# Kernel optimization log

Measured on AMD Instinct MI355X. Metric: run time of the kernel, lower is better.

The kernel has to match this reference:

```python
import jax, jax.numpy as jnp
import numpy as np

N_NODES = 50000
N_EDGES = 800000
NUM_GRAPHS = 256
H = 128          # h_dim
C = H + 1        # CGConv channels = 129
Z = 2 * C + 1    # concat(x_i, x_j, edge_attr) = 259
N_GRAPH_LAYERS = 5
N_FC = 3
OUT_DIM = 1


def setup_inputs() -> dict:
    key = jax.random.key(0)
    ks = jax.random.split(key, 12)
    atoms = jax.random.randint(ks[0], (N_NODES,), 0, 119)
    pos = jax.random.normal(ks[1], (N_NODES, 3), dtype=jnp.float32)
    edge_index = jax.random.randint(ks[2], (2, N_EDGES), 0, N_NODES)
    batch = jnp.sort(jax.random.randint(ks[3], (N_NODES,), 0, NUM_GRAPHS))
    s = 0.05
    emb = jax.random.normal(ks[4], (119, H), dtype=jnp.float32)
    Wf = jax.random.normal(ks[5], (N_GRAPH_LAYERS, Z, C), dtype=jnp.float32) * s
    bf = jnp.zeros((N_GRAPH_LAYERS, C), dtype=jnp.float32)
    Ws = jax.random.normal(ks[6], (N_GRAPH_LAYERS, Z, C), dtype=jnp.float32) * s
    bs = jnp.zeros((N_GRAPH_LAYERS, C), dtype=jnp.float32)
    Wfc = jax.random.normal(ks[7], (N_FC, C, C), dtype=jnp.float32) * s
    bfc = jnp.zeros((N_FC, C), dtype=jnp.float32)
    Wout = jax.random.normal(ks[8], (C, OUT_DIM), dtype=jnp.float32) * s
    bout = jnp.zeros((OUT_DIM,), dtype=jnp.float32)
    return {"atoms": atoms, "pos": pos, "edge_index": edge_index, "batch": batch,
            "emb": emb, "Wf": Wf, "bf": bf, "Ws": Ws, "bs": bs,
            "Wfc": Wfc, "bfc": bfc, "Wout": Wout, "bout": bout}


def reference(atoms, pos, edge_index, batch, emb, Wf, bf, Ws, bs, Wfc, bfc, Wout, bout):
    n = atoms.shape[0]
    src, dst = edge_index[0], edge_index[1]  # PyG: x_j = x[src], x_i = x[dst], aggregate at dst
    # edge_attr = ||pos[src] - pos[dst]||, shape [E, 1]
    edge_attr = jnp.linalg.norm(pos[src] - pos[dst], axis=-1, keepdims=True)
    # node features: atom embedding + z-coordinate -> [N, 129]
    x = jnp.concatenate([emb[atoms], pos[:, 2:3]], axis=-1)
    for l in range(Wf.shape[0]):
        z = jnp.concatenate([x[dst], x[src], edge_attr], axis=-1)  # [E, 259]
        m = jax.nn.sigmoid(z @ Wf[l] + bf[l]) * jax.nn.softplus(z @ Ws[l] + bs[l])
        x = x + jax.ops.segment_sum(m, dst, num_segments=n)  # CGConv: aggr='add' + residual
    # mean pooling per graph
    sums = jax.ops.segment_sum(x, batch, num_segments=NUM_GRAPHS)
    cnts = jax.ops.segment_sum(jnp.ones((n, 1), x.dtype), batch, num_segments=NUM_GRAPHS)
    g = sums / jnp.maximum(cnts, 1.0)
    for l in range(Wfc.shape[0]):
        g = g @ Wfc[l] + bfc[l]
    return g @ Wout + bout
```

## Files before the change

### kernel.cpp

```cpp
#include <hip/hip_runtime.h>
#include <math.h>

#define N_NODES 50000
#define N_EDGES 800000
#define NUM_GRAPHS 256
#define NPADROWS 50048
#define CAP 64
#define SCLN -1.44269504088896f
#define SCLP 1.44269504088896f
#define C693 0.69314718056f
#define LROW 264

typedef __attribute__((ext_vector_type(8))) short short8;
typedef __attribute__((ext_vector_type(4))) float f32x4;
typedef __attribute__((ext_vector_type(2))) float f32x2;

__device__ __forceinline__ float fast_rcp(float x) {
#if __has_builtin(__builtin_amdgcn_rcpf)
  return __builtin_amdgcn_rcpf(x);
#else
  return 1.0f / x;
#endif
}
__device__ __forceinline__ float EX2(float x) {
#if __has_builtin(__builtin_amdgcn_exp2f)
  return __builtin_amdgcn_exp2f(x);
#else
  return exp2f(x);
#endif
}
__device__ __forceinline__ float LG2(float x) {
#if __has_builtin(__builtin_amdgcn_logf)
  return __builtin_amdgcn_logf(x);
#else
  return log2f(x);
#endif
}
__device__ __forceinline__ unsigned f2bf(float x) {
  unsigned u = __float_as_uint(x);
  return (u + 0x7fffu + ((u >> 16) & 1u)) >> 16;
}
__device__ __forceinline__ unsigned short bfr(float v) {
  return (unsigned short)((__float_as_uint(v) + 0x8000u) >> 16);
}
__device__ __forceinline__ unsigned pkbfr(float lo, float hi) {
  unsigned a = (__float_as_uint(lo) + 0x8000u) >> 16;
  unsigned b = (__float_as_uint(hi) + 0x8000u) & 0xffff0000u;
  return a | b;
}
__device__ __forceinline__ float u2f(unsigned u) { return __uint_as_float(u); }
__device__ __forceinline__ f32x2 mk2(float a, float b) {
  f32x2 r; r.x = a; r.y = b; return r;
}
__device__ __forceinline__ f32x2 unp(unsigned u) {
  return mk2(u2f(u << 16), u2f(u & 0xffff0000u));
}
__device__ __forceinline__ f32x2 lg2p1(f32x2 t) {
  f32x2 p = __builtin_elementwise_fma(t, (f32x2)0.0439245f, (f32x2)-0.1898214f);
  p = __builtin_elementwise_fma(t, p, (f32x2)0.4115517f);
  p = __builtin_elementwise_fma(t, p, (f32x2)-0.7072504f);
  p = __builtin_elementwise_fma(t, p, (f32x2)1.4415927f);
  return t * p;
}
__device__ __forceinline__ void edge_ch2(f32x2 gf, f32x2 gs, f32x2& acc) {
  f32x2 den = mk2(EX2(gf.x), EX2(gf.y)) + 1.0f;
  f32x2 ts = mk2(EX2(-fabsf(gs.x)), EX2(-fabsf(gs.y)));
  f32x2 sp = lg2p1(ts) + __builtin_elementwise_max(gs, (f32x2)0.0f);
  f32x2 rc = mk2(fast_rcp(den.x), fast_rcp(den.y));
  acc = __builtin_elementwise_fma(rc, sp, acc);
}

__global__ void init_x(const int* __restrict__ atoms, const float* __restrict__ pos,
                       const float* __restrict__ emb, float* __restrict__ x128c,
                       unsigned* __restrict__ xbu, float4* __restrict__ pos4,
                       int* __restrict__ cnt) {
  int n = blockIdx.x;
  int t = threadIdx.x;
  int a = atoms[n];
  float2 e = *(const float2*)(emb + (size_t)a * 128 + 2 * t);
  xbu[(size_t)n * 64 + t] = f2bf(e.x) | (f2bf(e.y) << 16);
  if (t == 0) x128c[n] = pos[n * 3 + 2];
  if (t == 1) pos4[n] = make_float4(pos[3 * n], pos[3 * n + 1], pos[3 * n + 2], 0.f);
  if (t == 2) cnt[n] = 0;
}

__global__ void prep_b(const float* __restrict__ Wf, const float* __restrict__ Ws,
                       const float* __restrict__ bfp, const float* __restrict__ bsp,
                       uint4* __restrict__ Bp, float2* __restrict__ Wtail) {
  int idx = blockIdx.x * 256 + threadIdx.x;
  if (idx < 5 * 4 * 9 * 4 * 64) {
    int lane = idx & 63;
    int t = idx >> 6;
    int ks = t & 3; t >>= 2;
    int ct = t % 9; t /= 9;
    int g = t & 3;
    int l = t >> 2;
    const float* W = (g >= 2) ? Ws : Wf;
    float sc = (g < 2) ? SCLN : SCLP;
    int col = ct * 16 + (lane & 15);
    int kb = ks * 32 + (lane >> 4) * 8;
    unsigned u[4];
#pragma unroll
    for (int p = 0; p < 4; ++p) {
      unsigned lo = 0, hi = 0;
      if (col < 129) {
        int k0 = kb + 2 * p, k1 = k0 + 1;
        int r0 = (g & 1) ? 129 + k0 : k0;
        int r1 = (g & 1) ? 129 + k1 : k1;
        lo = f2bf(sc * W[(size_t)(l * 259 + r0) * 129 + col]);
        hi = f2bf(sc * W[(size_t)(l * 259 + r1) * 129 + col]);
      }
      u[p] = lo | (hi << 16);
    }
    Bp[idx] = make_uint4(u[0], u[1], u[2], u[3]);
  } else {
    int j = idx - 5 * 4 * 9 * 4 * 64;
    if (j >= 5 * 4 * 144) return;
    int c = j % 144;
    int t = j / 144;
    int g = t & 3;
    int l = t >> 2;
    float sc = (g < 2) ? SCLN : SCLP;
    float w1 = 0.0f, bias = 0.0f;
    if (c <= 128) {
      const float* W = (g >= 2) ? Ws : Wf;
      int row = (g & 1) ? 257 : 128;
      w1 = sc * W[(size_t)(l * 259 + row) * 129 + c];
      if (g == 0) bias = SCLN * bfp[l * 129 + c];
      if (g == 2) bias = SCLP * bsp[l * 129 + c];
    }
    Wtail[(l * 4 + g) * 144 + c] = make_float2(w1, bias);
  }
}

__global__ void build_csr(const int* __restrict__ ei, const float4* __restrict__ pos4,
                          const int* __restrict__ batch, int* __restrict__ cnt,
                          int2* __restrict__ csr, int* __restrict__ goff) {
  int e = blockIdx.x * 256 + threadIdx.x;
  if (e <= N_NODES) {
    int b = (e < N_NODES) ? batch[e] : NUM_GRAPHS;
    int bp = (e > 0) ? batch[e - 1] : -1;
    for (int g = bp + 1; g <= b; ++g) goff[g] = e;
  }
  if (e >= N_EDGES) return;
  int s = ei[e];
  int d = ei[N_EDGES + e];
  float4 ps = pos4[s];
  float4 pd = pos4[d];
  float dx = ps.x - pd.x, dy = ps.y - pd.y, dz = ps.z - pd.z;
  float ea = sqrtf(dx * dx + dy * dy + dz * dz);
  int p = atomicAdd(&cnt[d], 1);
  if (p < CAP) csr[d * CAP + p] = make_int2(s, __float_as_int(ea));
}

__global__ __launch_bounds__(256) void gemm_mfma(
    const unsigned* __restrict__ xbu, const float* __restrict__ x128c,
    const uint4* __restrict__ Bp, const float2* __restrict__ Wtail,
    unsigned short* __restrict__ Pdh, unsigned short* __restrict__ Pfs,
    unsigned* __restrict__ Pd128c, unsigned* __restrict__ Pc128, int layer) {
  __shared__ short smA[32 * 136];
  __shared__ unsigned short ldsD[32 * LROW];
  __shared__ unsigned short ldsS[32 * LROW];
  int n0 = blockIdx.x * 32;
  int tid = threadIdx.x;
  int g = tid >> 6;
  int l = tid & 63;
  int q = l >> 4, c16 = l & 15;
  const short8* Bp8 = (const short8*)Bp;
  const short8* Bq = Bp8 + (size_t)((layer * 4 + g) * 36) * 64 + l;

  int row0 = tid >> 4, cq = tid & 15;
  uint4 st0 = *(const uint4*)(xbu + (size_t)(n0 + row0) * 64 + cq * 4);
  uint4 st1 = *(const uint4*)(xbu + (size_t)(n0 + 16 + row0) * 64 + cq * 4);
  short8 b[9];
#pragma unroll
  for (int ct = 0; ct < 9; ++ct) b[ct] = Bq[(size_t)(ct * 4) * 64];
  *(uint4*)(&smA[row0 * 136 + cq * 8]) = st0;
  *(uint4*)(&smA[(16 + row0) * 136 + cq * 8]) = st1;
  __syncthreads();

  f32x4 acc[2][9];
#pragma unroll
  for (int rt = 0; rt < 2; ++rt)
#pragma unroll
    for (int ct = 0; ct < 9; ++ct) acc[rt][ct] = (f32x4){0.f, 0.f, 0.f, 0.f};
#pragma unroll
  for (int ks = 0; ks < 4; ++ks) {
    short8 a0 = *(const short8*)(&smA[c16 * 136 + (ks * 4 + q) * 8]);
    short8 a1 = *(const short8*)(&smA[(16 + c16) * 136 + (ks * 4 + q) * 8]);
    short8 bn[9];
    if (ks < 3) {
#pragma unroll
      for (int ct = 0; ct < 9; ++ct) bn[ct] = Bq[(size_t)(ct * 4 + ks + 1) * 64];
    }
#pragma unroll
    for (int ct = 0; ct < 9; ++ct) {
      acc[0][ct] = __builtin_amdgcn_mfma_f32_16x16x32_bf16(a0, b[ct], acc[0][ct], 0, 0, 0);
      acc[1][ct] = __builtin_amdgcn_mfma_f32_16x16x32_bf16(a1, b[ct], acc[1][ct], 0, 0, 0);
    }
    if (ks < 3) {
#pragma unroll
      for (int ct = 0; ct < 9; ++ct) b[ct] = bn[ct];
    }
  }
  const float2* Wt = Wtail + (layer * 4 + g) * 144;
  float x128[2][4];
#pragma unroll
  for (int rt = 0; rt < 2; ++rt)
#pragma unroll
    for (int r = 0; r < 4; ++r)
      x128[rt][r] = x128c[n0 + rt * 16 + q * 4 + r];
  unsigned short* ldsO = (g & 1) ? ldsS : ldsD;
  int soff = (g >= 2) ? 2 : 0;
  unsigned short* c128p = (g & 1) ? (unsigned short*)Pc128 : (unsigned short*)Pd128c;
  int c128o = (g >= 2) ? 1 : 0;
#pragma unroll
  for (int ct = 0; ct < 9; ++ct) {
    int col = ct * 16 + c16;
    float2 wb = Wt[col];
#pragma unroll
    for (int rt = 0; rt < 2; ++rt) {
#pragma unroll
      for (int r = 0; r < 4; ++r) {
        int rl = rt * 16 + q * 4 + r;
        float v = acc[rt][ct][r] + fmaf(x128[rt][r], wb.x, wb.y);
        if (col < 128) {
          ldsO[rl * LROW + ((col >> 1) << 2) + soff + (col & 1)] = bfr(v);
        } else if (col == 128) {
          c128p[2 * (size_t)(n0 + rl) + c128o] = bfr(v);
        }
      }
    }
  }
  __syncthreads();
#pragma unroll
  for (int i = tid; i < 2048; i += 256) {
    int img = i >> 10;
    int c = i & 1023;
    int row = c >> 5, part = c & 31;
    const unsigned short* src = (img ? ldsS : ldsD) + row * LROW + part * 8;
    unsigned short* dst = (img ? Pfs : Pdh) + (size_t)(n0 + row) * 256 + part * 8;
    *(uint4*)dst = *(const uint4*)src;
  }
}

__global__ __launch_bounds__(256) void edge_agg(
    const unsigned short* __restrict__ Pdh, const unsigned short* __restrict__ Pfs,
    const unsigned* __restrict__ Pd128c, const unsigned* __restrict__ Pc128,
    unsigned* __restrict__ xbu, float* __restrict__ x128c, const int* __restrict__ cnt,
    const int2* __restrict__ csr, const float* __restrict__ WfL,
    const float* __restrict__ WsL) {
  int lane = threadIdx.x & 63;
  int half = lane >> 5;
  int l5 = lane & 31;
  int n = blockIdx.x * 4 + (threadIdx.x >> 6);
  if (n >= N_NODES) return;
  int nu = __builtin_amdgcn_readfirstlane(n);
  const float* wfl = WfL + 258 * 129;
  const float* wsl = WsL + 258 * 129;
  uint4 pdv = *(const uint4*)(Pdh + (size_t)nu * 256 + 8 * l5);
  f32x2 bfa = unp(pdv.x), bsa = unp(pdv.y), bfb = unp(pdv.z), bsb = unp(pdv.w);
  float2 wfa0 = *(const float2*)(wfl + 4 * l5);
  float2 wfb0 = *(const float2*)(wfl + 4 * l5 + 2);
  float2 wsa0 = *(const float2*)(wsl + 4 * l5);
  float2 wsb0 = *(const float2*)(wsl + 4 * l5 + 2);
  f32x2 wfa = mk2(SCLN * wfa0.x, SCLN * wfa0.y), wfb = mk2(SCLN * wfb0.x, SCLN * wfb0.y);
  f32x2 wsa = mk2(SCLP * wsa0.x, SCLP * wsa0.y), wsb = mk2(SCLP * wsb0.x, SCLP * wsb0.y);
  unsigned pd1 = Pd128c[nu];
  float bfc8 = u2f(pd1 << 16), bsc8 = u2f(pd1 & 0xffff0000u);
  float wfc8 = SCLN * wfl[128], wsc8 = SCLP * wsl[128];
  int m = cnt[nu];
  if (m > CAP) m = CAP;
  const int4* cb4 = (const int4*)(csr + (size_t)nu * CAP);
  const uint4* Pfq = (const uint4*)Pfs;
  f32x2 accA = (f32x2)0.0f, accB = (f32x2)0.0f;

#define GATHER(qq) Pfq[(size_t)(half ? qq.z : qq.x) * 32 + l5]
#define COMPUTE(qq, gg)                                                       \
  {                                                                           \
    f32x2 ea_ = (f32x2)__int_as_float(half ? qq.w : qq.y);                    \
    edge_ch2(__builtin_elementwise_fma(ea_, wfa, bfa + unp(gg.x)),            \
             __builtin_elementwise_fma(ea_, wsa, bsa + unp(gg.y)), accA);     \
    edge_ch2(__builtin_elementwise_fma(ea_, wfb, bfb + unp(gg.z)),            \
             __builtin_elementwise_fma(ea_, wsb, bsb + unp(gg.w)), accB);     \
  }

  int Pf = m >> 1;
  int4 qc = make_int4(0, 0, 0, 0);
  uint4 gc = make_uint4(0, 0, 0, 0);
  if (Pf > 0) {
    qc = cb4[0];
    gc = GATHER(qc);
  }
  for (int p = 0; p < Pf; ++p) {
    int4 qn = qc;
    uint4 gn = gc;
    if (p + 1 < Pf) {
      qn = cb4[p + 1];
      gn = GATHER(qn);
    }
    COMPUTE(qc, gc);
    qc = qn;
    gc = gn;
  }
  if ((m & 1) && half == 0) {
    int4 qt = cb4[Pf];
    f32x2 ea_ = (f32x2)__int_as_float(qt.y);
    uint4 gt = Pfq[(size_t)qt.x * 32 + l5];
    edge_ch2(__builtin_elementwise_fma(ea_, wfa, bfa + unp(gt.x)),
             __builtin_elementwise_fma(ea_, wsa, bsa + unp(gt.y)), accA);
    edge_ch2(__builtin_elementwise_fma(ea_, wfb, bfb + unp(gt.z)),
             __builtin_elementwise_fma(ea_, wsb, bsb + unp(gt.w)), accB);
  }
#undef GATHER
#undef COMPUTE

  accA.x += __shfl_xor(accA.x, 32, 64);
  accA.y += __shfl_xor(accA.y, 32, 64);
  accB.x += __shfl_xor(accB.x, 32, 64);
  accB.y += __shfl_xor(accB.y, 32, 64);

  float v2 = 0.f;
  if (lane < m) {
    int2 se = csr[(size_t)nu * CAP + lane];
    float ea = __int_as_float(se.y);
    unsigned pc = Pc128[se.x];
    float f2 = u2f(pc << 16), s2 = u2f(pc & 0xffff0000u);
    float gf2 = fmaf(ea, wfc8, bfc8 + f2);
    float gs2 = fmaf(ea, wsc8, bsc8 + s2);
    float sp2 = LG2(1.0f + EX2(-fabsf(gs2))) + fmaxf(gs2, 0.0f);
    v2 = C693 * fast_rcp(1.0f + EX2(gf2)) * sp2;
  }
#pragma unroll
  for (int off = 32; off; off >>= 1) v2 += __shfl_down(v2, off, 64);

  if (half == 0) {
    uint2 xv = *(const uint2*)(xbu + (size_t)nu * 64 + 2 * l5);
    f32x2 xa = __builtin_elementwise_fma(accA, (f32x2)C693, unp(xv.x));
    f32x2 xb = __builtin_elementwise_fma(accB, (f32x2)C693, unp(xv.y));
    *(uint2*)(xbu + (size_t)nu * 64 + 2 * l5) =
        make_uint2(pkbfr(xa.x, xa.y), pkbfr(xb.x, xb.y));
  }
  if (lane == 0) x128c[nu] += v2;
}

__global__ void pool2(const unsigned* __restrict__ xbu, const float* __restrict__ x128c,
                      const int* __restrict__ goff, float* __restrict__ gpart) {
  int gph = blockIdx.x >> 2;
  int q = blockIdx.x & 3;
  int t = threadIdx.x;
  if (t >= 129) return;
  int s = goff[gph], e = goff[gph + 1];
  int len = e - s;
  int chunk = (len + 3) >> 2;
  int a = s + q * chunk;
  int b = a + chunk; if (b > e) b = e;
  float acc = 0.f;
  if (t < 128) {
    int w = t >> 1, hi = t & 1;
    for (int n = a; n < b; ++n) {
      unsigned u = xbu[(size_t)n * 64 + w];
      acc += hi ? u2f(u & 0xffff0000u) : u2f(u << 16);
    }
  } else {
    for (int n = a; n < b; ++n) acc += x128c[n];
  }
  gpart[(size_t)(gph * 4 + q) * 132 + t] = acc;
}

__global__ void fcout(const float* __restrict__ gpart, const int* __restrict__ goff,
                      const float* __restrict__ Wfc, const float* __restrict__ bfc,
                      const float* __restrict__ Wout, const float* __restrict__ bout,
                      float* __restrict__ out) {
  __shared__ float buf[2][132];
  __shared__ float red[3];
  int i = blockIdx.x;
  int t = threadIdx.x;
  bool act = t < 129;
  int len = goff[i + 1] - goff[i];
  float inv = fast_rcp(fmaxf((float)len, 1.0f));
  if (act) {
    float v = gpart[(size_t)(i * 4 + 0) * 132 + t] + gpart[(size_t)(i * 4 + 1) * 132 + t] +
              gpart[(size_t)(i * 4 + 2) * 132 + t] + gpart[(size_t)(i * 4 + 3) * 132 + t];
    buf[0][t] = v * inv;
  }
  __syncthreads();
  int cur = 0;
#pragma unroll
  for (int l = 0; l < 3; ++l) {
    float s = 0.f;
    if (act) {
      const float* Wl = Wfc + (size_t)l * 129 * 129 + t;
      s = bfc[l * 129 + t];
      float wA[16], wB[16];
      float wlast = Wl[(size_t)128 * 129];
#pragma unroll
      for (int j = 0; j < 16; ++j) wA[j] = Wl[(size_t)j * 129];
#pragma unroll
      for (int kb = 0; kb < 128; kb += 16) {
        const int gidx = kb >> 4;
        float* wc = (gidx & 1) ? wB : wA;
        float* wn = (gidx & 1) ? wA : wB;
        if (kb + 16 < 128) {
#pragma unroll
          for (int j = 0; j < 16; ++j) wn[j] = Wl[(size_t)(kb + 16 + j) * 129];
        }
#pragma unroll
        for (int j = 0; j < 16; ++j) s = fmaf(buf[cur][kb + j], wc[j], s);
      }
      s = fmaf(buf[cur][128], wlast, s);
    }
    __syncthreads();
    if (act) buf[1 - cur][t] = s;
    cur = 1 - cur;
    __syncthreads();
  }
  float p = act ? buf[cur][t] * Wout[t] : 0.f;
#pragma unroll
  for (int off = 32; off; off >>= 1) p += __shfl_down(p, off, 64);
  if ((t & 63) == 0) red[t >> 6] = p;
  __syncthreads();
  if (t == 0) out[i] = red[0] + red[1] + red[2] + bout[0];
}

extern "C" void kernel_launch(void* const* d_in, const int* in_sizes, int n_in,
                              void* d_out, int out_size, void* d_ws, size_t ws_size,
                              hipStream_t stream) {
  const int* atoms = (const int*)d_in[0];
  const float* pos = (const float*)d_in[1];
  const int* ei = (const int*)d_in[2];
  const int* batch = (const int*)d_in[3];
  const float* emb = (const float*)d_in[4];
  const float* Wf = (const float*)d_in[5];
  const float* bfp = (const float*)d_in[6];
  const float* Ws = (const float*)d_in[7];
  const float* bsp = (const float*)d_in[8];
  const float* Wfc = (const float*)d_in[9];
  const float* bfc = (const float*)d_in[10];
  const float* Wout = (const float*)d_in[11];
  const float* bout = (const float*)d_in[12];
  float* outp = (float*)d_out;

  uint4* Bp = (uint4*)d_ws;
  unsigned* xbu = (unsigned*)(Bp + 46080);
  unsigned short* Pdh = (unsigned short*)(xbu + (size_t)NPADROWS * 64);
  unsigned short* Pfs = Pdh + (size_t)NPADROWS * 256;
  float4* pos4 = (float4*)(Pfs + (size_t)NPADROWS * 256);
  float2* Wtail = (float2*)(pos4 + N_NODES);
  float* x128c = (float*)(Wtail + 5 * 4 * 144);
  float* gpart = x128c + NPADROWS;
  int* goff = (int*)(gpart + 256 * 4 * 132);
  int* cnt = goff + 260;
  int2* csr = (int2*)(cnt + N_NODES + 4);
  unsigned* Pd128c = (unsigned*)(csr + (size_t)N_NODES * CAP);
  unsigned* Pc128 = Pd128c + NPADROWS;

  init_x<<<N_NODES, 64, 0, stream>>>(atoms, pos, emb, x128c, xbu, pos4, cnt);
  prep_b<<<(5 * 4 * 9 * 4 * 64 + 5 * 4 * 144 + 255) / 256, 256, 0, stream>>>(
      Wf, Ws, bfp, bsp, Bp, Wtail);
  build_csr<<<(N_EDGES + 255) / 256, 256, 0, stream>>>(ei, pos4, batch, cnt, csr, goff);

  for (int l = 0; l < 5; ++l) {
    gemm_mfma<<<NPADROWS / 32, 256, 0, stream>>>(xbu, x128c, Bp, Wtail, Pdh, Pfs,
                                                 Pd128c, Pc128, l);
    edge_agg<<<(N_NODES + 3) / 4, 256, 0, stream>>>(Pdh, Pfs, Pd128c, Pc128, xbu, x128c,
                                                    cnt, csr,
                                                    Wf + (size_t)l * 259 * 129,
                                                    Ws + (size_t)l * 259 * 129);
  }

  pool2<<<NUM_GRAPHS * 4, 192, 0, stream>>>(xbu, x128c, goff, gpart);
  fcout<<<NUM_GRAPHS, 192, 0, stream>>>(gpart, goff, Wfc, bfc, Wout, bout, outp);
}
```

Measured before the change: 622.5 us.

## Sort nodes by in-degree so edge aggregation waves get balanced work

Adds a histogram, a descending scan and a scatter that build a permutation of nodes ordered by capped in-degree. The edge aggregation kernel maps each wavefront to perm[widx], so the four waves in a block handle nodes of similar degree and the heavy nodes are scheduled first. This targets load imbalance and tail effects, since degrees follow a Poisson distribution with mean 16. In exchange it adds three small kernels and an indirect lookup, and it loses the locality that came from processing node rows sequentially.

Result: slower. 901.4 us (+44.8%).

```diff
diff --git a/kernel.cpp b/kernel.cpp
--- a/kernel.cpp
+++ b/kernel.cpp
@@ -73,7 +73,7 @@
 __global__ void init_x(const int* __restrict__ atoms, const float* __restrict__ pos,
                        const float* __restrict__ emb, float* __restrict__ x128c,
                        unsigned* __restrict__ xbu, float4* __restrict__ pos4,
-                       int* __restrict__ cnt) {
+                       int* __restrict__ cnt, int* __restrict__ hh) {
   int n = blockIdx.x;
   int t = threadIdx.x;
   int a = atoms[n];
@@ -82,6 +82,10 @@
   if (t == 0) x128c[n] = pos[n * 3 + 2];
   if (t == 1) pos4[n] = make_float4(pos[3 * n], pos[3 * n + 1], pos[3 * n + 2], 0.f);
   if (t == 2) cnt[n] = 0;
+  if (n == 0) {
+    hh[t] = 0;
+    if (t == 0) hh[64] = 0;
+  }
 }
 
 __global__ void prep_b(const float* __restrict__ Wf, const float* __restrict__ Ws,
@@ -153,6 +157,32 @@
   if (p < CAP) csr[d * CAP + p] = make_int2(s, __float_as_int(ea));
 }
 
+__global__ void deg_hist(const int* __restrict__ cnt, int* __restrict__ hh) {
+  int n = blockIdx.x * 256 + threadIdx.x;
+  if (n >= N_NODES) return;
+  int d = cnt[n]; if (d > CAP) d = CAP;
+  atomicAdd(&hh[d], 1);
+}
+__global__ void deg_scan(const int* __restrict__ hh, int* __restrict__ hcur) {
+  __shared__ int sh[CAP + 1];
+  int t = threadIdx.x;
+  if (t <= CAP) sh[t] = hh[t];
+  __syncthreads();
+  if (t <= CAP) {
+    int run = 0;
+    for (int d = CAP; d > t; --d) run += sh[d];
+    hcur[t] = run;
+  }
+}
+__global__ void deg_scatter(const int* __restrict__ cnt, int* __restrict__ hcur,
+                            int* __restrict__ perm) {
+  int n = blockIdx.x * 256 + threadIdx.x;
+  if (n >= N_NODES) return;
+  int d = cnt[n]; if (d > CAP) d = CAP;
+  int pos = atomicAdd(&hcur[d], 1);
+  perm[pos] = n;
+}
+
 __global__ __launch_bounds__(256) void gemm_mfma(
     const unsigned* __restrict__ xbu, const float* __restrict__ x128c,
     const uint4* __restrict__ Bp, const float2* __restrict__ Wtail,
@@ -249,13 +279,13 @@
     const unsigned* __restrict__ Pd128c, const unsigned* __restrict__ Pc128,
     unsigned* __restrict__ xbu, float* __restrict__ x128c, const int* __restrict__ cnt,
     const int2* __restrict__ csr, const float* __restrict__ WfL,
-    const float* __restrict__ WsL) {
+    const float* __restrict__ WsL, const int* __restrict__ perm) {
   int lane = threadIdx.x & 63;
   int half = lane >> 5;
   int l5 = lane & 31;
-  int n = blockIdx.x * 4 + (threadIdx.x >> 6);
-  if (n >= N_NODES) return;
-  int nu = __builtin_amdgcn_readfirstlane(n);
+  int widx = blockIdx.x * 4 + (threadIdx.x >> 6);
+  if (widx >= N_NODES) return;
+  int nu = __builtin_amdgcn_readfirstlane(perm[widx]);
   const float* wfl = WfL + 258 * 129;
   const float* wsl = WsL + 258 * 129;
   uint4 pdv = *(const uint4*)(Pdh + (size_t)nu * 256 + 8 * l5);
@@ -454,11 +484,17 @@
   int2* csr = (int2*)(cnt + N_NODES + 4);
   unsigned* Pd128c = (unsigned*)(csr + (size_t)N_NODES * CAP);
   unsigned* Pc128 = Pd128c + NPADROWS;
-
-  init_x<<<N_NODES, 64, 0, stream>>>(atoms, pos, emb, x128c, xbu, pos4, cnt);
+  int* perm = (int*)(Pc128 + NPADROWS);
+  int* hh = perm + N_NODES;
+  int* hcur = hh + 68;
+
+  init_x<<<N_NODES, 64, 0, stream>>>(atoms, pos, emb, x128c, xbu, pos4, cnt, hh);
   prep_b<<<(5 * 4 * 9 * 4 * 64 + 5 * 4 * 144 + 255) / 256, 256, 0, stream>>>(
       Wf, Ws, bfp, bsp, Bp, Wtail);
   build_csr<<<(N_EDGES + 255) / 256, 256, 0, stream>>>(ei, pos4, batch, cnt, csr, goff);
+  deg_hist<<<(N_NODES + 255) / 256, 256, 0, stream>>>(cnt, hh);
+  deg_scan<<<1, 128, 0, stream>>>(hh, hcur);
+  deg_scatter<<<(N_NODES + 255) / 256, 256, 0, stream>>>(cnt, hcur, perm);
 
   for (int l = 0; l < 5; ++l) {
     gemm_mfma<<<NPADROWS / 32, 256, 0, stream>>>(xbu, x128c, Bp, Wtail, Pdh, Pfs,
@@ -466,7 +502,7 @@
     edge_agg<<<(N_NODES + 3) / 4, 256, 0, stream>>>(Pdh, Pfs, Pd128c, Pc128, xbu, x128c,
                                                     cnt, csr,
                                                     Wf + (size_t)l * 259 * 129,
-                                                    Ws + (size_t)l * 259 * 129);
+                                                    Ws + (size_t)l * 259 * 129, perm);
   }
 
   pool2<<<NUM_GRAPHS * 4, 192, 0, stream>>>(xbu, x128c, goff, gpart);
```

## Sort nodes by in-degree so edge_agg processes similar-degree nodes together

Applied to the files above, without the earlier changes.

Adds three small kernels that build a per-block degree histogram, compute offsets, and scatter node ids into a permutation ordered from high degree to low. edge_agg then maps each wavefront to perm[widx] instead of the node index. The aim is to balance work across wavefronts in a block and schedule heavy nodes first, reducing tail imbalance from variable degree. It costs three extra launches and an indirection, and loses the sequential node locality for Pdh and xbu accesses.

Result: no change. 624.2 us (+0.3%).

```diff
diff --git a/kernel.cpp b/kernel.cpp
--- a/kernel.cpp
+++ b/kernel.cpp
@@ -6,6 +6,8 @@
 #define NUM_GRAPHS 256
 #define NPADROWS 50048
 #define CAP 64
+#define NHB 64
+#define DCH ((N_NODES + NHB - 1) / NHB)
 #define SCLN -1.44269504088896f
 #define SCLP 1.44269504088896f
 #define C693 0.69314718056f
@@ -153,6 +155,55 @@
   if (p < CAP) csr[d * CAP + p] = make_int2(s, __float_as_int(ea));
 }
 
+__global__ void deg_hist_blk(const int* __restrict__ cnt, int* __restrict__ bcnt) {
+  __shared__ int sh[CAP + 1];
+  int t = threadIdx.x, b = blockIdx.x;
+  if (t <= CAP) sh[t] = 0;
+  __syncthreads();
+  int a = b * DCH, e = a + DCH;
+  if (e > N_NODES) e = N_NODES;
+  for (int n = a + t; n < e; n += 256) {
+    int d = cnt[n]; if (d > CAP) d = CAP;
+    atomicAdd(&sh[d], 1);
+  }
+  __syncthreads();
+  if (t <= CAP) bcnt[b * (CAP + 1) + t] = sh[t];
+}
+__global__ void deg_off(const int* __restrict__ bcnt, int* __restrict__ boff) {
+  __shared__ int tot[CAP + 1];
+  int d = threadIdx.x;
+  int c[NHB];
+  if (d <= CAP) {
+#pragma unroll
+    for (int b = 0; b < NHB; ++b) c[b] = bcnt[b * (CAP + 1) + d];
+    int run = 0;
+#pragma unroll
+    for (int b = 0; b < NHB; ++b) { int v = c[b]; c[b] = run; run += v; }
+    tot[d] = run;
+  }
+  __syncthreads();
+  if (d <= CAP) {
+    int gbase = 0;
+    for (int dd = d + 1; dd <= CAP; ++dd) gbase += tot[dd];
+#pragma unroll
+    for (int b = 0; b < NHB; ++b) boff[b * (CAP + 1) + d] = c[b] + gbase;
+  }
+}
+__global__ void deg_scatter_blk(const int* __restrict__ cnt,
+                                const int* __restrict__ boff, int* __restrict__ perm) {
+  __shared__ int base[CAP + 1];
+  int t = threadIdx.x, b = blockIdx.x;
+  if (t <= CAP) base[t] = boff[b * (CAP + 1) + t];
+  __syncthreads();
+  int a = b * DCH, e = a + DCH;
+  if (e > N_NODES) e = N_NODES;
+  for (int n = a + t; n < e; n += 256) {
+    int d = cnt[n]; if (d > CAP) d = CAP;
+    int pos = atomicAdd(&base[d], 1);
+    perm[pos] = n;
+  }
+}
+
 __global__ __launch_bounds__(256) void gemm_mfma(
     const unsigned* __restrict__ xbu, const float* __restrict__ x128c,
     const uint4* __restrict__ Bp, const float2* __restrict__ Wtail,
@@ -249,13 +300,13 @@
     const unsigned* __restrict__ Pd128c, const unsigned* __restrict__ Pc128,
     unsigned* __restrict__ xbu, float* __restrict__ x128c, const int* __restrict__ cnt,
     const int2* __restrict__ csr, const float* __restrict__ WfL,
-    const float* __restrict__ WsL) {
+    const float* __restrict__ WsL, const int* __restrict__ perm) {
   int lane = threadIdx.x & 63;
   int half = lane >> 5;
   int l5 = lane & 31;
-  int n = blockIdx.x * 4 + (threadIdx.x >> 6);
-  if (n >= N_NODES) return;
-  int nu = __builtin_amdgcn_readfirstlane(n);
+  int widx = blockIdx.x * 4 + (threadIdx.x >> 6);
+  if (widx >= N_NODES) return;
+  int nu = __builtin_amdgcn_readfirstlane(perm[widx]);
   const float* wfl = WfL + 258 * 129;
   const float* wsl = WsL + 258 * 129;
   uint4 pdv = *(const uint4*)(Pdh + (size_t)nu * 256 + 8 * l5);
@@ -454,11 +505,17 @@
   int2* csr = (int2*)(cnt + N_NODES + 4);
   unsigned* Pd128c = (unsigned*)(csr + (size_t)N_NODES * CAP);
   unsigned* Pc128 = Pd128c + NPADROWS;
+  int* perm = (int*)(Pc128 + NPADROWS);
+  int* bcnt = perm + N_NODES;
+  int* boff = bcnt + NHB * (CAP + 1);
 
   init_x<<<N_NODES, 64, 0, stream>>>(atoms, pos, emb, x128c, xbu, pos4, cnt);
   prep_b<<<(5 * 4 * 9 * 4 * 64 + 5 * 4 * 144 + 255) / 256, 256, 0, stream>>>(
       Wf, Ws, bfp, bsp, Bp, Wtail);
   build_csr<<<(N_EDGES + 255) / 256, 256, 0, stream>>>(ei, pos4, batch, cnt, csr, goff);
+  deg_hist_blk<<<NHB, 256, 0, stream>>>(cnt, bcnt);
+  deg_off<<<1, 128, 0, stream>>>(bcnt, boff);
+  deg_scatter_blk<<<NHB, 256, 0, stream>>>(cnt, boff, perm);
 
   for (int l = 0; l < 5; ++l) {
     gemm_mfma<<<NPADROWS / 32, 256, 0, stream>>>(xbu, x128c, Bp, Wtail, Pdh, Pfs,
@@ -466,7 +523,7 @@
     edge_agg<<<(N_NODES + 3) / 4, 256, 0, stream>>>(Pdh, Pfs, Pd128c, Pc128, xbu, x128c,
                                                     cnt, csr,
                                                     Wf + (size_t)l * 259 * 129,
-                                                    Ws + (size_t)l * 259 * 129);
+                                                    Ws + (size_t)l * 259 * 129, perm);
   }
 
   pool2<<<NUM_GRAPHS * 4, 192, 0, stream>>>(xbu, x128c, goff, gpart);
```
